# Kernel optimization log

Measured on AMD Instinct MI355X. Metric: run time of the kernel, lower is better.

## Reference

```python
import jax, jax.numpy as jnp
import numpy as np

M = 7            # window size
N = M * M        # tokens per window = 49
HEADS = 8
DIM = 256
NW = 64          # windows per image (56x56 feature map / 7x7 windows)
B_WIN = 4096     # B * num_windows (batch 64 images)


def _relative_position_index():
    # Standard Swin relative position index, shape (N, N), values in [0, (2M-1)^2)
    coords = np.stack(np.meshgrid(np.arange(M), np.arange(M), indexing='ij'))  # (2,M,M)
    coords = coords.reshape(2, -1)                                             # (2,N)
    rel = coords[:, :, None] - coords[:, None, :]                              # (2,N,N)
    rel = rel.transpose(1, 2, 0).astype(np.int32)                              # (N,N,2)
    rel[..., 0] += M - 1
    rel[..., 1] += M - 1
    rel[..., 0] *= 2 * M - 1
    return rel.sum(-1)  # (N,N)


def setup_inputs() -> dict:
    key = jax.random.key(0)
    ks = jax.random.split(key, 7)
    x = jax.random.normal(ks[0], (B_WIN, N, DIM), dtype=jnp.float32)
    # Shifted-window attention mask: 0 where attend, -100 where blocked
    mask = jnp.where(jax.random.uniform(ks[1], (NW, N, N)) > 0.5, 0.0, -100.0).astype(jnp.float32)
    rel_index = jnp.asarray(_relative_position_index(), dtype=jnp.int32)
    qkv_w = jax.random.normal(ks[2], (3 * DIM, DIM), dtype=jnp.float32) * 0.02
    qkv_b = jax.random.normal(ks[3], (3 * DIM,), dtype=jnp.float32) * 0.02
    proj_w = jax.random.normal(ks[4], (DIM, DIM), dtype=jnp.float32) * 0.02
    proj_b = jax.random.normal(ks[5], (DIM,), dtype=jnp.float32) * 0.02
    bias_table = jax.random.normal(ks[6], ((2 * M - 1) ** 2, HEADS), dtype=jnp.float32) * 0.02
    return {"x": x, "mask": mask, "rel_index": rel_index, "qkv_w": qkv_w,
            "qkv_b": qkv_b, "proj_w": proj_w, "proj_b": proj_b, "bias_table": bias_table}


def reference(x, mask, rel_index, qkv_w, qkv_b, proj_w, proj_b, bias_table):
    B, n, C = x.shape                      # (B*nW, 49, 256)
    h = bias_table.shape[1]
    d = C // h
    scale = d ** -0.5
    # qkv projection -> (3, B, h, n, d)
    qkv = (x @ qkv_w.T + qkv_b).reshape(B, n, 3, h, d).transpose(2, 0, 3, 1, 4)
    q, k, v = qkv[0] * scale, qkv[1], qkv[2]
    attn = jnp.einsum('bhnd,bhmd->bhnm', q, k)              # (B,h,n,n)
    # relative position bias gather: (n,n) index into (169,h) -> (h,n,n)
    bias = bias_table[rel_index].transpose(2, 0, 1)
    attn = attn + bias[None]
    # per-window mask: attn viewed as (B//nW, nW, h, n, n) + mask (nW,1,n,n)
    nW = mask.shape[0]
    attn = attn.reshape(B // nW, nW, h, n, n) + mask[None, :, None]
    attn = jax.nn.softmax(attn.reshape(B, h, n, n), axis=-1)
    out = jnp.einsum('bhnm,bhmd->bhnd', attn, v)            # (B,h,n,d)
    out = out.transpose(0, 2, 1, 3).reshape(B, n, C)
    return out @ proj_w.T + proj_b
```

## Files before the change

kernel.cpp:

```cpp
#include <hip/hip_runtime.h>
#include <cstdint>


typedef __attribute__((ext_vector_type(8))) short short8;
typedef __attribute__((ext_vector_type(4))) float floatx4;

__device__ __forceinline__ ushort f2bf(float f) {
    uint32_t u = __float_as_uint(f);
    u += 0x7FFFu + ((u >> 16) & 1u);
    return (ushort)(u >> 16);
}

__device__ __forceinline__ uint32_t cvtpk(float lo, float hi) {
    uint32_t r;
    asm("v_cvt_pk_bf16_f32 %0, %1, %2" : "=v"(r) : "v"(lo), "v"(hi));
    return r;
}

__global__ __launch_bounds__(256) void k_cvt_w(const float* __restrict__ qw,
                                               const float* __restrict__ pw,
                                               ushort* __restrict__ qwb,
                                               ushort* __restrict__ pwb) {
    int i = blockIdx.x * 256 + threadIdx.x;
    if (i < 196608) qwb[i] = f2bf(qw[i]);
    else            pwb[i - 196608] = f2bf(pw[i - 196608]);
}

__global__ __launch_bounds__(256) void k_comb(const float* __restrict__ mask,
                                              const int* __restrict__ rel,
                                              const float* __restrict__ bt,
                                              float* __restrict__ comb) {
    const int wh = blockIdx.x;
    const int w = wh >> 3, h = wh & 7;
    const float* mw = mask + (size_t)w * 2401;
    float* out = comb + (size_t)wh * 4096;
    for (int e = threadIdx.x; e < 49 * 64; e += 256) {
        const int n = e >> 6, m = e & 63;
        out[e] = (m < 49) ? mw[n * 49 + m] + bt[rel[n * 49 + m] * 8 + h] : 0.0f;
    }
}

__global__ __launch_bounds__(512, 2) void k_mono(
        const ushort* __restrict__ qwb, const float* __restrict__ x,
        const float* __restrict__ qb, const float* __restrict__ comb,
        const ushort* __restrict__ pwb, const float* __restrict__ pb,
        float* __restrict__ out) {
    __shared__ ushort smem[38912];
    ushort* xb = smem;

    const int t = threadIdx.x;
    const int w = t >> 6, l = t & 63;
    const int g = l >> 4, li = l & 15;
    const int blk = blockIdx.x;
    const int wdw = blk & 63;

    ushort* scr = smem + w * 4864;
    ushort* vtw = smem + w * 4864 + 2560;
    ushort* P   = smem + w * 4864;
    ushort* ao  = smem;

    {
        const int n = t >> 3, seg = t & 7;
        if (n < 49) {
            const float* src = x + ((size_t)blk * 49 + n) * 256 + seg * 32;
#pragma unroll
            for (int c4 = 0; c4 < 4; ++c4) {
                const float4 a  = *(const float4*)(src + c4 * 8);
                const float4 b2 = *(const float4*)(src + c4 * 8 + 4);
                uint4 u;
                u.x = cvtpk(a.x, a.y);  u.y = cvtpk(a.z, a.w);
                u.z = cvtpk(b2.x, b2.y); u.w = cvtpk(b2.z, b2.w);
                const int j = seg * 4 + c4;
                *(uint4*)(xb + n * 256 + ((j ^ (n & 7)) * 8)) = u;
            }
        } else {
            const uint4 z = {0u, 0u, 0u, 0u};
#pragma unroll
            for (int c4 = 0; c4 < 4; ++c4) {
                const int j = seg * 4 + c4;
                *(uint4*)(xb + n * 256 + ((j ^ (n & 7)) * 8)) = z;
            }
        }
    }
    __syncthreads();

    const floatx4 zf = {0.f, 0.f, 0.f, 0.f};
    const float scale = 0.17677669529663687f;

    const int rowbase[6] = {w * 32,       w * 32 + 16,
                            256 + w * 32, 256 + w * 32 + 16,
                            512 + w * 32, 512 + w * 32 + 16};
    floatx4 acc[6][4];
#pragma unroll
    for (int i = 0; i < 6; ++i)
#pragma unroll
        for (int j = 0; j < 4; ++j) acc[i][j] = zf;

#pragma unroll
    for (int kt = 0; kt < 8; ++kt) {
        short8 af[6], bfr[4];
#pragma unroll
        for (int ct = 0; ct < 6; ++ct)
            af[ct] = *(const short8*)(qwb +
                (size_t)(rowbase[ct] + li) * 256 + kt * 32 + g * 8);
#pragma unroll
        for (int nt = 0; nt < 4; ++nt)
            bfr[nt] = *(const short8*)(xb + (nt * 16 + li) * 256 +
                (((kt * 4 + g) ^ (li & 7)) * 8));
#pragma unroll
        for (int ct = 0; ct < 6; ++ct)
#pragma unroll
            for (int nt = 0; nt < 4; ++nt)
                acc[ct][nt] = __builtin_amdgcn_mfma_f32_16x16x32_bf16(
                    af[ct], bfr[nt], acc[ct][nt], 0, 0, 0);
    }
    __syncthreads();

    short8 qf[4], kf[4], vf[2][2];

#pragma unroll
    for (int ct = 0; ct < 2; ++ct) {
        const int dd0 = ct * 16 + g * 4;
        const float4 b4 = *(const float4*)(qb + w * 32 + dd0);
#pragma unroll
        for (int nt = 0; nt < 4; ++nt) {
            const int n = nt * 16 + li;
            uint2 pk2;
            pk2.x = cvtpk(acc[ct][nt][0] + b4.x, acc[ct][nt][1] + b4.y);
            pk2.y = cvtpk(acc[ct][nt][2] + b4.z, acc[ct][nt][3] + b4.w);
            *(uint2*)(scr + n * 40 + dd0) = pk2;
        }
    }
#pragma unroll
    for (int mt = 0; mt < 4; ++mt)
        qf[mt] = *(const short8*)(scr + (mt * 16 + li) * 40 + g * 8);

#pragma unroll
    for (int ct = 2; ct < 4; ++ct) {
        const int dd0 = (ct - 2) * 16 + g * 4;
        const float4 b4 = *(const float4*)(qb + 256 + w * 32 + dd0);
#pragma unroll
        for (int nt = 0; nt < 4; ++nt) {
            const int n = nt * 16 + li;
            uint2 pk2;
            pk2.x = cvtpk(acc[ct][nt][0] + b4.x, acc[ct][nt][1] + b4.y);
            pk2.y = cvtpk(acc[ct][nt][2] + b4.z, acc[ct][nt][3] + b4.w);
            *(uint2*)(scr + n * 40 + dd0) = pk2;
        }
    }
#pragma unroll
    for (int mt = 0; mt < 4; ++mt)
        kf[mt] = *(const short8*)(scr + (mt * 16 + li) * 40 + g * 8);

#pragma unroll
    for (int ct = 4; ct < 6; ++ct) {
        const int dd0 = (ct - 4) * 16 + g * 4;
        const float4 b4 = *(const float4*)(qb + 512 + w * 32 + dd0);
#pragma unroll
        for (int nt = 0; nt < 4; ++nt) {
            const int n = nt * 16 + li;
            vtw[(dd0 + 0) * 72 + n] = f2bf(acc[ct][nt][0] + b4.x);
            vtw[(dd0 + 1) * 72 + n] = f2bf(acc[ct][nt][1] + b4.y);
            vtw[(dd0 + 2) * 72 + n] = f2bf(acc[ct][nt][2] + b4.z);
            vtw[(dd0 + 3) * 72 + n] = f2bf(acc[ct][nt][3] + b4.w);
        }
    }
#pragma unroll
    for (int ks = 0; ks < 2; ++ks)
#pragma unroll
        for (int nt = 0; nt < 2; ++nt)
            vf[ks][nt] = *(const short8*)(vtw + (nt * 16 + li) * 72 +
                                          ks * 32 + g * 8);

    floatx4 sac[4][4];
#pragma unroll
    for (int bq = 0; bq < 4; ++bq)
#pragma unroll
        for (int ak = 0; ak < 4; ++ak)
            sac[bq][ak] = __builtin_amdgcn_mfma_f32_16x16x32_bf16(
                kf[ak], qf[bq], zf, 0, 0, 0);

    const float* cw = comb + (size_t)(wdw * 8 + w) * 4096;

#pragma unroll
    for (int bq = 0; bq < 4; ++bq) {
        const int n = bq * 16 + li;
        const float* cr = cw + n * 64 + g * 4;
        const float4 c0 = *(const float4*)(cr);
        const float4 c1 = *(const float4*)(cr + 16);
        const float4 c2 = *(const float4*)(cr + 32);
        const float c3x = cr[48];
        float v[12];
        v[0]  = sac[bq][0][0] * scale + c0.x;
        v[1]  = sac[bq][0][1] * scale + c0.y;
        v[2]  = sac[bq][0][2] * scale + c0.z;
        v[3]  = sac[bq][0][3] * scale + c0.w;
        v[4]  = sac[bq][1][0] * scale + c1.x;
        v[5]  = sac[bq][1][1] * scale + c1.y;
        v[6]  = sac[bq][1][2] * scale + c1.z;
        v[7]  = sac[bq][1][3] * scale + c1.w;
        v[8]  = sac[bq][2][0] * scale + c2.x;
        v[9]  = sac[bq][2][1] * scale + c2.y;
        v[10] = sac[bq][2][2] * scale + c2.z;
        v[11] = sac[bq][2][3] * scale + c2.w;
        const float v48 = (g == 0) ? sac[bq][3][0] * scale + c3x : -3.0e38f;
        float mx = fmaxf(fmaxf(fmaxf(v[0], v[1]), fmaxf(v[2], v[3])),
                         fmaxf(fmaxf(v[4], v[5]), fmaxf(v[6], v[7])));
        mx = fmaxf(mx, fmaxf(fmaxf(v[8], v[9]), fmaxf(v[10], v[11])));
        mx = fmaxf(mx, v48);
        mx = fmaxf(mx, __shfl_xor(mx, 16, 64));
        mx = fmaxf(mx, __shfl_xor(mx, 32, 64));
        float e[12], s = 0.f;
#pragma unroll
        for (int i = 0; i < 12; ++i) { e[i] = __expf(v[i] - mx); s += e[i]; }
        const float e48 = __expf(v48 - mx);
        s += e48;
        s += __shfl_xor(s, 16, 64);
        s += __shfl_xor(s, 32, 64);
        const float inv = 1.0f / s;
        uint2 pk;
#pragma unroll
        for (int a = 0; a < 3; ++a) {
            pk.x = cvtpk(e[a * 4 + 0] * inv, e[a * 4 + 1] * inv);
            pk.y = cvtpk(e[a * 4 + 2] * inv, e[a * 4 + 3] * inv);
            *(uint2*)(P + n * 72 + a * 16 + g * 4) = pk;
        }
        pk.x = cvtpk(e48 * inv, 0.f);
        pk.y = 0u;
        *(uint2*)(P + n * 72 + 48 + g * 4) = pk;
    }

    floatx4 oac[4][2];
#pragma unroll
    for (int mt = 0; mt < 4; ++mt)
#pragma unroll
        for (int nt = 0; nt < 2; ++nt) oac[mt][nt] = zf;
#pragma unroll
    for (int ks = 0; ks < 2; ++ks)
#pragma unroll
        for (int mt = 0; mt < 4; ++mt) {
            const short8 pf = *(const short8*)(P + (mt * 16 + li) * 72 +
                                               ks * 32 + g * 8);
            oac[mt][0] = __builtin_amdgcn_mfma_f32_16x16x32_bf16(
                pf, vf[ks][0], oac[mt][0], 0, 0, 0);
            oac[mt][1] = __builtin_amdgcn_mfma_f32_16x16x32_bf16(
                pf, vf[ks][1], oac[mt][1], 0, 0, 0);
        }

    __syncthreads();

#pragma unroll
    for (int mt = 0; mt < 4; ++mt)
#pragma unroll
        for (int rr = 0; rr < 4; ++rr) {
            const int n = mt * 16 + g * 4 + rr;
            if (n < 49) {
#pragma unroll
                for (int nt = 0; nt < 2; ++nt)
                    ao[n * 264 + w * 32 + nt * 16 + li] = f2bf(oac[mt][nt][rr]);
            }
        }
    for (int idx = l; idx < 240; idx += 64) {
        const int n = 49 + (idx >> 4);
        const int du = idx & 15;
        *(uint32_t*)(ao + n * 264 + w * 32 + du * 2) = 0u;
    }
    __syncthreads();

    floatx4 pacc[4][2];
#pragma unroll
    for (int mt = 0; mt < 4; ++mt)
#pragma unroll
        for (int nt = 0; nt < 2; ++nt) pacc[mt][nt] = zf;
#pragma unroll
    for (int kt = 0; kt < 8; ++kt) {
        short8 afr[4], wfr[2];
#pragma unroll
        for (int mt = 0; mt < 4; ++mt)
            afr[mt] = *(const short8*)(ao + (mt * 16 + li) * 264 + kt * 32 + g * 8);
#pragma unroll
        for (int nt = 0; nt < 2; ++nt)
            wfr[nt] = *(const short8*)(pwb +
                (size_t)(w * 32 + nt * 16 + li) * 256 + kt * 32 + g * 8);
#pragma unroll
        for (int mt = 0; mt < 4; ++mt)
#pragma unroll
            for (int nt = 0; nt < 2; ++nt)
                pacc[mt][nt] = __builtin_amdgcn_mfma_f32_16x16x32_bf16(
                    afr[mt], wfr[nt], pacc[mt][nt], 0, 0, 0);
    }

    float* og = out + (size_t)blk * 49 * 256;
#pragma unroll
    for (int nt = 0; nt < 2; ++nt) {
        const int c = w * 32 + nt * 16 + li;
        const float bias = pb[c];
#pragma unroll
        for (int mt = 0; mt < 4; ++mt)
#pragma unroll
            for (int r = 0; r < 4; ++r) {
                const int n = mt * 16 + g * 4 + r;
                if (n < 49) og[(size_t)n * 256 + c] = pacc[mt][nt][r] + bias;
            }
    }
}

extern "C" void kernel_launch(void* const* d_in, const int* in_sizes, int n_in,
                              void* d_out, int out_size, void* d_ws, size_t ws_size,
                              hipStream_t stream) {
    const float* x      = (const float*)d_in[0];
    const float* mask   = (const float*)d_in[1];
    const int*   rel    = (const int*)d_in[2];
    const float* qkv_w  = (const float*)d_in[3];
    const float* qkv_b  = (const float*)d_in[4];
    const float* proj_w = (const float*)d_in[5];
    const float* proj_b = (const float*)d_in[6];
    const float* bt     = (const float*)d_in[7];
    float* out = (float*)d_out;

    char* ws = (char*)d_ws;
    ushort* qwb  = (ushort*)(ws);
    ushort* pwb  = (ushort*)(ws + 393216);
    float*  comb = (float*) (ws + 524288);
    (void)ws_size; (void)in_sizes; (void)n_in; (void)out_size;

    k_cvt_w<<<dim3(1024), dim3(256), 0, stream>>>(qkv_w, proj_w, qwb, pwb);
    k_comb <<<dim3(512),  dim3(256), 0, stream>>>(mask, rel, bt, comb);
    k_mono <<<dim3(4096), dim3(512), 0, stream>>>(qwb, x, qkv_b, comb, pwb,
                                                  proj_b, out);
}
```

Measured before the change: 411.5 us.

## Split QKV GEMM into three passes reading x directly from global memory

Drops the shared-memory staging of the bf16 window input. The QKV projection now runs as three sequential passes (V, then Q, then K), each holding only 2x4 accumulators, and converts x fragments from global fp32 straight into MFMA operands. The score MFMAs are also moved inside the per-row softmax loop, and launch bounds are raised to ask for 4 blocks per CU. The aim is lower register pressure and higher occupancy, but the same x rows are now fetched and converted three times per block, and the ~78KB static LDS allocation likely still caps residency at 2 blocks per CU.

```diff
diff --git a/kernel.cpp b/kernel.cpp
--- a/kernel.cpp
+++ b/kernel.cpp
@@ -40,13 +40,12 @@
     }
 }
 
-__global__ __launch_bounds__(512, 2) void k_mono(
+__global__ __launch_bounds__(512, 4) void k_mono(
         const ushort* __restrict__ qwb, const float* __restrict__ x,
         const float* __restrict__ qb, const float* __restrict__ comb,
         const ushort* __restrict__ pwb, const float* __restrict__ pb,
         float* __restrict__ out) {
     __shared__ ushort smem[38912];
-    ushort* xb = smem;
 
     const int t = threadIdx.x;
     const int w = t >> 6, l = t & 63;
@@ -59,65 +58,67 @@
     ushort* P   = smem + w * 4864;
     ushort* ao  = smem;
 
-    {
-        const int n = t >> 3, seg = t & 7;
-        if (n < 49) {
-            const float* src = x + ((size_t)blk * 49 + n) * 256 + seg * 32;
-#pragma unroll
-            for (int c4 = 0; c4 < 4; ++c4) {
-                const float4 a  = *(const float4*)(src + c4 * 8);
-                const float4 b2 = *(const float4*)(src + c4 * 8 + 4);
-                uint4 u;
-                u.x = cvtpk(a.x, a.y);  u.y = cvtpk(a.z, a.w);
-                u.z = cvtpk(b2.x, b2.y); u.w = cvtpk(b2.z, b2.w);
-                const int j = seg * 4 + c4;
-                *(uint4*)(xb + n * 256 + ((j ^ (n & 7)) * 8)) = u;
-            }
-        } else {
-            const uint4 z = {0u, 0u, 0u, 0u};
-#pragma unroll
-            for (int c4 = 0; c4 < 4; ++c4) {
-                const int j = seg * 4 + c4;
-                *(uint4*)(xb + n * 256 + ((j ^ (n & 7)) * 8)) = z;
-            }
-        }
-    }
-    __syncthreads();
-
     const floatx4 zf = {0.f, 0.f, 0.f, 0.f};
+    const short8 z8 = {0, 0, 0, 0, 0, 0, 0, 0};
     const float scale = 0.17677669529663687f;
-
-    const int rowbase[6] = {w * 32,       w * 32 + 16,
-                            256 + w * 32, 256 + w * 32 + 16,
-                            512 + w * 32, 512 + w * 32 + 16};
-    floatx4 acc[6][4];
-#pragma unroll
-    for (int i = 0; i < 6; ++i)
-#pragma unroll
-        for (int j = 0; j < 4; ++j) acc[i][j] = zf;
-
-#pragma unroll
-    for (int kt = 0; kt < 8; ++kt) {
-        short8 af[6], bfr[4];
-#pragma unroll
-        for (int ct = 0; ct < 6; ++ct)
-            af[ct] = *(const short8*)(qwb +
-                (size_t)(rowbase[ct] + li) * 256 + kt * 32 + g * 8);
-#pragma unroll
-        for (int nt = 0; nt < 4; ++nt)
-            bfr[nt] = *(const short8*)(xb + (nt * 16 + li) * 256 +
-                (((kt * 4 + g) ^ (li & 7)) * 8));
-#pragma unroll
-        for (int ct = 0; ct < 6; ++ct)
-#pragma unroll
-            for (int nt = 0; nt < 4; ++nt)
-                acc[ct][nt] = __builtin_amdgcn_mfma_f32_16x16x32_bf16(
-                    af[ct], bfr[nt], acc[ct][nt], 0, 0, 0);
-    }
-    __syncthreads();
-
-    short8 qf[4], kf[4], vf[2][2];
-
+    const float* xw = x + (size_t)blk * 49 * 256;
+
+    auto load_bx = [&](int nt, int kt) -> short8 {
+        const int n = nt * 16 + li;
+        if (n >= 49) return z8;
+        const float* p = xw + (size_t)n * 256 + kt * 32 + g * 8;
+        const float4 a = *(const float4*)p;
+        const float4 b = *(const float4*)(p + 4);
+        union { short8 s; uint32_t u[4]; } cv;
+        cv.u[0] = cvtpk(a.x, a.y);
+        cv.u[1] = cvtpk(a.z, a.w);
+        cv.u[2] = cvtpk(b.x, b.y);
+        cv.u[3] = cvtpk(b.z, b.w);
+        return cv.s;
+    };
+
+    floatx4 acc[2][4];
+
+#define GEMM_PASS(BASE)                                                       \
+    {                                                                         \
+        _Pragma("unroll")                                                     \
+        for (int i = 0; i < 2; ++i)                                           \
+            _Pragma("unroll")                                                 \
+            for (int j = 0; j < 4; ++j) acc[i][j] = zf;                       \
+        _Pragma("unroll")                                                     \
+        for (int kt = 0; kt < 8; ++kt) {                                      \
+            short8 af0 = *(const short8*)(qwb +                               \
+                (size_t)((BASE) + li) * 256 + kt * 32 + g * 8);               \
+            short8 af1 = *(const short8*)(qwb +                               \
+                (size_t)((BASE) + 16 + li) * 256 + kt * 32 + g * 8);          \
+            _Pragma("unroll")                                                 \
+            for (int nt = 0; nt < 4; ++nt) {                                  \
+                const short8 bx = load_bx(nt, kt);                            \
+                acc[0][nt] = __builtin_amdgcn_mfma_f32_16x16x32_bf16(         \
+                    af0, bx, acc[0][nt], 0, 0, 0);                            \
+                acc[1][nt] = __builtin_amdgcn_mfma_f32_16x16x32_bf16(         \
+                    af1, bx, acc[1][nt], 0, 0, 0);                            \
+            }                                                                 \
+        }                                                                     \
+    }
+
+    GEMM_PASS(512 + w * 32)
+#pragma unroll
+    for (int ct = 0; ct < 2; ++ct) {
+        const int dd0 = ct * 16 + g * 4;
+        const float4 b4 = *(const float4*)(qb + 512 + w * 32 + dd0);
+#pragma unroll
+        for (int nt = 0; nt < 4; ++nt) {
+            const int n = nt * 16 + li;
+            vtw[(dd0 + 0) * 72 + n] = f2bf(acc[ct][nt][0] + b4.x);
+            vtw[(dd0 + 1) * 72 + n] = f2bf(acc[ct][nt][1] + b4.y);
+            vtw[(dd0 + 2) * 72 + n] = f2bf(acc[ct][nt][2] + b4.z);
+            vtw[(dd0 + 3) * 72 + n] = f2bf(acc[ct][nt][3] + b4.w);
+        }
+    }
+
+    short8 qf[4], kf[4];
+    GEMM_PASS(w * 32)
 #pragma unroll
     for (int ct = 0; ct < 2; ++ct) {
         const int dd0 = ct * 16 + g * 4;
@@ -135,9 +136,10 @@
     for (int mt = 0; mt < 4; ++mt)
         qf[mt] = *(const short8*)(scr + (mt * 16 + li) * 40 + g * 8);
 
-#pragma unroll
-    for (int ct = 2; ct < 4; ++ct) {
-        const int dd0 = (ct - 2) * 16 + g * 4;
+    GEMM_PASS(256 + w * 32)
+#pragma unroll
+    for (int ct = 0; ct < 2; ++ct) {
+        const int dd0 = ct * 16 + g * 4;
         const float4 b4 = *(const float4*)(qb + 256 + w * 32 + dd0);
 #pragma unroll
         for (int nt = 0; nt < 4; ++nt) {
@@ -152,19 +154,7 @@
     for (int mt = 0; mt < 4; ++mt)
         kf[mt] = *(const short8*)(scr + (mt * 16 + li) * 40 + g * 8);
 
-#pragma unroll
-    for (int ct = 4; ct < 6; ++ct) {
-        const int dd0 = (ct - 4) * 16 + g * 4;
-        const float4 b4 = *(const float4*)(qb + 512 + w * 32 + dd0);
-#pragma unroll
-        for (int nt = 0; nt < 4; ++nt) {
-            const int n = nt * 16 + li;
-            vtw[(dd0 + 0) * 72 + n] = f2bf(acc[ct][nt][0] + b4.x);
-            vtw[(dd0 + 1) * 72 + n] = f2bf(acc[ct][nt][1] + b4.y);
-            vtw[(dd0 + 2) * 72 + n] = f2bf(acc[ct][nt][2] + b4.z);
-            vtw[(dd0 + 3) * 72 + n] = f2bf(acc[ct][nt][3] + b4.w);
-        }
-    }
+    short8 vf[2][2];
 #pragma unroll
     for (int ks = 0; ks < 2; ++ks)
 #pragma unroll
@@ -172,18 +162,16 @@
             vf[ks][nt] = *(const short8*)(vtw + (nt * 16 + li) * 72 +
                                           ks * 32 + g * 8);
 
-    floatx4 sac[4][4];
-#pragma unroll
-    for (int bq = 0; bq < 4; ++bq)
+    const float* cw = comb + (size_t)(wdw * 8 + w) * 4096;
+
+#pragma unroll
+    for (int bq = 0; bq < 4; ++bq) {
+        floatx4 sac[4];
 #pragma unroll
         for (int ak = 0; ak < 4; ++ak)
-            sac[bq][ak] = __builtin_amdgcn_mfma_f32_16x16x32_bf16(
+            sac[ak] = __builtin_amdgcn_mfma_f32_16x16x32_bf16(
                 kf[ak], qf[bq], zf, 0, 0, 0);
 
-    const float* cw = comb + (size_t)(wdw * 8 + w) * 4096;
-
-#pragma unroll
-    for (int bq = 0; bq < 4; ++bq) {
         const int n = bq * 16 + li;
         const float* cr = cw + n * 64 + g * 4;
         const float4 c0 = *(const float4*)(cr);
@@ -191,19 +179,19 @@
         const float4 c2 = *(const float4*)(cr + 32);
         const float c3x = cr[48];
         float v[12];
-        v[0]  = sac[bq][0][0] * scale + c0.x;
-        v[1]  = sac[bq][0][1] * scale + c0.y;
-        v[2]  = sac[bq][0][2] * scale + c0.z;
-        v[3]  = sac[bq][0][3] * scale + c0.w;
-        v[4]  = sac[bq][1][0] * scale + c1.x;
-        v[5]  = sac[bq][1][1] * scale + c1.y;
-        v[6]  = sac[bq][1][2] * scale + c1.z;
-        v[7]  = sac[bq][1][3] * scale + c1.w;
-        v[8]  = sac[bq][2][0] * scale + c2.x;
-        v[9]  = sac[bq][2][1] * scale + c2.y;
-        v[10] = sac[bq][2][2] * scale + c2.z;
-        v[11] = sac[bq][2][3] * scale + c2.w;
-        const float v48 = (g == 0) ? sac[bq][3][0] * scale + c3x : -3.0e38f;
+        v[0]  = sac[0][0] * scale + c0.x;
+        v[1]  = sac[0][1] * scale + c0.y;
+        v[2]  = sac[0][2] * scale + c0.z;
+        v[3]  = sac[0][3] * scale + c0.w;
+        v[4]  = sac[1][0] * scale + c1.x;
+        v[5]  = sac[1][1] * scale + c1.y;
+        v[6]  = sac[1][2] * scale + c1.z;
+        v[7]  = sac[1][3] * scale + c1.w;
+        v[8]  = sac[2][0] * scale + c2.x;
+        v[9]  = sac[2][1] * scale + c2.y;
+        v[10] = sac[2][2] * scale + c2.z;
+        v[11] = sac[2][3] * scale + c2.w;
+        const float v48 = (g == 0) ? sac[3][0] * scale + c3x : -3.0e38f;
         float mx = fmaxf(fmaxf(fmaxf(v[0], v[1]), fmaxf(v[2], v[3])),
                          fmaxf(fmaxf(v[4], v[5]), fmaxf(v[6], v[7])));
         mx = fmaxf(mx, fmaxf(fmaxf(v[8], v[9]), fmaxf(v[10], v[11])));
@@ -303,6 +291,7 @@
                 if (n < 49) og[(size_t)n * 256 + c] = pacc[mt][nt][r] + bias;
             }
     }
+#undef GEMM_PASS
 }
 
 extern "C" void kernel_launch(void* const* d_in, const int* in_sizes, int n_in,
```

Result: slower. 875.5 us (+112.8%).
